# Kernel optimization log

Hardware: AMD Instinct MI355X
Metric: run time of the kernel (lower is better)

The kernel has to match this reference:

```python
import jax, jax.numpy as jnp
import numpy as np

# FUME epipolar image translation: for each output pixel p2=(x2,y2) the fundamental
# matrix F maps it to a line l = F @ [x2*d, y2*d, 1] in the input view (full-res
# coordinates; d = per-batch downsampling factor). The output value is the line
# integral of the input image along that epipolar line, computed by stepping one
# pixel at a time along the dominant axis with bilinear (1-D linear) interpolation
# across the other axis; out-of-bounds samples contribute zero.

def _translate(img, F, d):
    B, C, H, W = img.shape
    dt = img.dtype
    yy, xx = jnp.meshgrid(jnp.arange(H, dtype=dt), jnp.arange(W, dtype=dt), indexing='ij')
    db = d[:, None, None].astype(dt)                          # (B,1,1)
    px, py = xx[None] * db, yy[None] * db                     # (B,H,W) full-res coords
    a = F[0, 0] * px + F[0, 1] * py + F[0, 2]                 # line coeffs l = F @ [x,y,1]
    b = F[1, 0] * px + F[1, 1] * py + F[1, 2]
    c = F[2, 0] * px + F[2, 1] * py + F[2, 2]
    horiz = jnp.abs(b) >= jnp.abs(a)                          # dominant axis per pixel

    db4 = db[..., None]                                       # (B,1,1,1)
    # horizontal traversal: step over columns s, solve a*(s*d) + b*(y*d) + c = 0
    s = jnp.arange(W, dtype=dt)
    denom_h = jnp.where(horiz, b, jnp.ones((), dt))[..., None] * db4
    yline = -(a[..., None] * (s * db4) + c[..., None]) / denom_h    # (B,H,W,W)
    # vertical traversal: step over rows t, solve for x
    t = jnp.arange(H, dtype=dt)
    denom_v = jnp.where(horiz, jnp.ones((), dt), a)[..., None] * db4
    xline = -(b[..., None] * (t * db4) + c[..., None]) / denom_v    # (B,H,W,H)

    def sample_one(imgb, y, x):
        # imgb: (C,H,W); y: (H,W,W) row coord per column step; x: (H,W,H) col coord per row step
        y0 = jnp.floor(y)
        wy = y - y0
        y0i = jnp.clip(y0.astype(jnp.int32), 0, H - 1)
        y1i = jnp.clip(y0i + 1, 0, H - 1)
        cols = jnp.arange(W)
        vh = (1 - wy)[None] * imgb[:, y0i, cols] + wy[None] * imgb[:, y1i, cols]  # (C,H,W,W)
        vh = jnp.where(((y >= 0) & (y <= H - 1))[None], vh, jnp.zeros((), imgb.dtype)).sum(-1)

        x0 = jnp.floor(x)
        wx = x - x0
        x0i = jnp.clip(x0.astype(jnp.int32), 0, W - 1)
        x1i = jnp.clip(x0i + 1, 0, W - 1)
        rows = jnp.arange(H)
        vv = (1 - wx)[None] * imgb[:, rows, x0i] + wx[None] * imgb[:, rows, x1i]  # (C,H,W,H)
        vv = jnp.where(((x >= 0) & (x <= W - 1))[None], vv, jnp.zeros((), imgb.dtype)).sum(-1)
        return vh, vv

    vh, vv = jax.vmap(sample_one)(img, yline, xline)          # each (B,C,H,W)
    return jnp.where(horiz[:, None], vh, vv)


def setup_inputs() -> dict:
    key = jax.random.key(0)
    k1, k2, k3 = jax.random.split(key, 3)
    B, C, H, W = 4, 4, 128, 128
    view1 = jax.random.normal(k1, (B, C, H, W), jnp.float32)
    F21 = jax.random.normal(k2, (3, 3), jnp.float32)
    F12 = jax.random.normal(k3, (3, 3), jnp.float32)
    downsampled_factor = jnp.ones((B,), jnp.float32)
    return {"view1": view1, "F21": F21, "F12": F12, "downsampled_factor": downsampled_factor}


def reference(view1, F21, F12, downsampled_factor):
    # forward uses F21 only; F12 is kept for the backward pass in the original module
    return _translate(view1, F21, downsampled_factor)
```

## Files before the change

### kernel.cpp

```cpp
#include <hip/hip_runtime.h>


#define CC 4
#define HH 128
#define WW 128
#define LDK 128
#define CUBE (128 * LDK)

typedef _Float16 h2 __attribute__((ext_vector_type(2)));

__global__ void __launch_bounds__(256) fume_stage(
        const float* __restrict__ img, float4* __restrict__ ws) {
    __shared__ float tile[4][17][17];
    int x0 = blockIdx.x * 16, y0 = blockIdx.y * 16, b = blockIdx.z;
    int tx = threadIdx.x, ty = threadIdx.y;
    int id = ty * 16 + tx;
    const float* src = img + (size_t)b * CC * HH * WW;

    #pragma unroll
    for (int ch = 0; ch < 4; ++ch) {
        #pragma unroll
        for (int e = 0; e < 2; ++e) {
            int idx = id + e * 256;
            if (idx < 289) {
                int i = idx / 17, j = idx % 17;
                int r = min(y0 + i, HH - 1);
                int c = min(x0 + j, WW - 1);
                tile[ch][i][j] = src[(ch * HH + r) * WW + c];
            }
        }
    }
    __syncthreads();

    float4* base_h = ws + (size_t)b * (2 * CUBE);
    float4* base_v = base_h + CUBE;

    {
        h2 p0 = { (_Float16)tile[0][ty][tx], (_Float16)tile[0][ty + 1][tx] };
        h2 p1 = { (_Float16)tile[1][ty][tx], (_Float16)tile[1][ty + 1][tx] };
        h2 p2 = { (_Float16)tile[2][ty][tx], (_Float16)tile[2][ty + 1][tx] };
        h2 p3 = { (_Float16)tile[3][ty][tx], (_Float16)tile[3][ty + 1][tx] };
        float4 e = make_float4(__builtin_bit_cast(float, p0),
                               __builtin_bit_cast(float, p1),
                               __builtin_bit_cast(float, p2),
                               __builtin_bit_cast(float, p3));
        base_h[(y0 + ty) * LDK + (x0 + tx)] = e;
    }
    {
        h2 p0 = { (_Float16)tile[0][tx][ty], (_Float16)tile[0][tx][ty + 1] };
        h2 p1 = { (_Float16)tile[1][tx][ty], (_Float16)tile[1][tx][ty + 1] };
        h2 p2 = { (_Float16)tile[2][tx][ty], (_Float16)tile[2][tx][ty + 1] };
        h2 p3 = { (_Float16)tile[3][tx][ty], (_Float16)tile[3][tx][ty + 1] };
        float4 e = make_float4(__builtin_bit_cast(float, p0),
                               __builtin_bit_cast(float, p1),
                               __builtin_bit_cast(float, p2),
                               __builtin_bit_cast(float, p3));
        base_v[(x0 + ty) * LDK + (y0 + tx)] = e;
    }
}

__global__ void __launch_bounds__(512) fume_kernel(
        const float4* __restrict__ cubes,
        const float* __restrict__ F,
        const float* __restrict__ dsf,
        float* __restrict__ out) {
    int j = threadIdx.x;
    int w = threadIdx.y;
    int x = blockIdx.x * 8 + w;
    int y = blockIdx.y;
    int b = blockIdx.z;

    float d = dsf[b];
    float F00 = F[0], F01 = F[1], F02 = F[2];
    float F10 = F[3], F11 = F[4], F12 = F[5];
    float F20 = F[6], F21 = F[7], F22 = F[8];

    float px = __fmul_rn((float)x, d);
    float py = __fmul_rn((float)y, d);
    float av = __fadd_rn(__fadd_rn(__fmul_rn(F00, px), __fmul_rn(F01, py)), F02);
    float bv = __fadd_rn(__fadd_rn(__fmul_rn(F10, px), __fmul_rn(F11, py)), F12);
    float cv = __fadd_rn(__fadd_rn(__fmul_rn(F20, px), __fmul_rn(F21, py)), F22);

    bool horiz  = fabsf(bv) >= fabsf(av);
    float ncoef = horiz ? av : bv;
    float den   = __fmul_rn(horiz ? bv : av, d);
    float nrec  = -__fdiv_rn(1.0f, den);

    const float4* P = cubes + (size_t)b * (2 * CUBE) + (horiz ? 0 : CUBE);

    float A  = __fmul_rn(__fmul_rn(ncoef, d), nrec);
    float Bc = __fmul_rn(cv, nrec);
    int lkmin, lkmax;
    if (fabsf(A) > 1e-20f) {
        float inv = 1.0f / A;
        float k1 = (0.0f   - Bc) * inv;
        float k2 = (127.0f - Bc) * inv;
        float lo = fmaxf(fminf(k1, k2) - 2.0f, 0.0f);
        float hi = fminf(fmaxf(k1, k2) + 2.0f, 127.0f);
        if (lo > hi || !(lo == lo)) { lkmin = 1; lkmax = 0; }
        else { lkmin = (int)lo; lkmax = (int)hi; }
    } else {
        bool full = (Bc >= 0.0f) && (Bc <= 127.0f);
        lkmin = full ? 0 : 1;
        lkmax = full ? 127 : 0;
    }

    float a0 = 0.f, a1 = 0.f, a2 = 0.f, a3 = 0.f;
    #pragma unroll
    for (int t = 0; t < 2; ++t) {
        int k = lkmin + (t << 6) + j;
        if (k <= lkmax) {
            float m  = __fmul_rn((float)k, d);
            float q  = __fadd_rn(__fmul_rn(ncoef, m), cv);
            float u  = __fmul_rn(q, nrec);
            bool ok  = (u >= 0.f) && (u <= 127.f);
            int i0   = (int)floorf(u);
            i0 = max(0, min(i0, 126));
            float wq = __fsub_rn(u, (float)i0);
            h2 wp = __builtin_bit_cast(h2,
                        __builtin_amdgcn_cvt_pkrtz(__fsub_rn(1.f, wq), wq));
            wp = ok ? wp : (h2){(_Float16)0.f, (_Float16)0.f};
            float4 e = P[i0 * LDK + k];
            a0 = __builtin_amdgcn_fdot2(wp, __builtin_bit_cast(h2, e.x), a0, false);
            a1 = __builtin_amdgcn_fdot2(wp, __builtin_bit_cast(h2, e.y), a1, false);
            a2 = __builtin_amdgcn_fdot2(wp, __builtin_bit_cast(h2, e.z), a2, false);
            a3 = __builtin_amdgcn_fdot2(wp, __builtin_bit_cast(h2, e.w), a3, false);
        }
    }

    #pragma unroll
    for (int mlt = 32; mlt >= 1; mlt >>= 1) {
        a0 = __fadd_rn(a0, __shfl_xor(a0, mlt));
        a1 = __fadd_rn(a1, __shfl_xor(a1, mlt));
        a2 = __fadd_rn(a2, __shfl_xor(a2, mlt));
        a3 = __fadd_rn(a3, __shfl_xor(a3, mlt));
    }

    if (j < 4) {
        float v = (j == 0) ? a0 : (j == 1) ? a1 : (j == 2) ? a2 : a3;
        out[(((size_t)b * CC + j) * HH + y) * WW + x] = v;
    }
}

extern "C" void kernel_launch(void* const* d_in, const int* in_sizes, int n_in,
                              void* d_out, int out_size, void* d_ws, size_t ws_size,
                              hipStream_t stream) {
    const float* view1 = (const float*)d_in[0];
    const float* F21   = (const float*)d_in[1];
    const float* dsf   = (const float*)d_in[3];

    const int B = in_sizes[3];

    dim3 stb(16, 16, 1);
    dim3 stg(WW / 16, HH / 16, B);
    fume_stage<<<stg, stb, 0, stream>>>(view1, (float4*)d_ws);

    dim3 ftb(64, 8, 1);
    dim3 ftg(WW / 8, HH, B);
    fume_kernel<<<ftg, ftb, 0, stream>>>((const float4*)d_ws, F21, dsf,
                                         (float*)d_out);
}
```

Baseline: 79.32 us.

## Map eight output pixels per wavefront with 8-lane sub-groups and adaptive step count

Each wavefront now handles eight output pixels, with eight lanes per pixel, instead of one pixel per 64-lane wavefront. The loop runs only as many steps as the longest clipped line segment in the wave needs, and the final reduction spans eight lanes instead of 64. This is meant to cut idle lanes on short clipped segments and to shorten the shuffle reduction. In exchange the loop now has a runtime trip count, and lanes whose segments are short sit idle while the longest segment in the wave finishes; gathers from eight lanes may also coalesce less well.

```diff
diff --git a/kernel.cpp b/kernel.cpp
--- a/kernel.cpp
+++ b/kernel.cpp
@@ -64,9 +64,11 @@
         const float* __restrict__ F,
         const float* __restrict__ dsf,
         float* __restrict__ out) {
-    int j = threadIdx.x;
-    int w = threadIdx.y;
-    int x = blockIdx.x * 8 + w;
+    int lane = threadIdx.x;
+    int sub  = lane & 7;
+    int oct  = lane >> 3;
+    int w    = threadIdx.y;
+    int x = blockIdx.x * 64 + w * 8 + oct;
     int y = blockIdx.y;
     int b = blockIdx.z;
 
@@ -105,10 +107,15 @@
         lkmax = full ? 127 : 0;
     }
 
+    int len = lkmax - lkmin + 1;
+    int cnt = (len + 7) >> 3;
+    int wm  = cnt;
+    #pragma unroll
+    for (int m = 1; m < 64; m <<= 1) wm = max(wm, __shfl_xor(wm, m));
+
     float a0 = 0.f, a1 = 0.f, a2 = 0.f, a3 = 0.f;
-    #pragma unroll
-    for (int t = 0; t < 2; ++t) {
-        int k = lkmin + (t << 6) + j;
+    for (int s = 0; s < wm; ++s) {
+        int k = lkmin + (s << 3) + sub;
         if (k <= lkmax) {
             float m  = __fmul_rn((float)k, d);
             float q  = __fadd_rn(__fmul_rn(ncoef, m), cv);
@@ -129,16 +136,16 @@
     }
 
     #pragma unroll
-    for (int mlt = 32; mlt >= 1; mlt >>= 1) {
-        a0 = __fadd_rn(a0, __shfl_xor(a0, mlt));
-        a1 = __fadd_rn(a1, __shfl_xor(a1, mlt));
-        a2 = __fadd_rn(a2, __shfl_xor(a2, mlt));
-        a3 = __fadd_rn(a3, __shfl_xor(a3, mlt));
+    for (int m = 1; m < 8; m <<= 1) {
+        a0 = __fadd_rn(a0, __shfl_xor(a0, m));
+        a1 = __fadd_rn(a1, __shfl_xor(a1, m));
+        a2 = __fadd_rn(a2, __shfl_xor(a2, m));
+        a3 = __fadd_rn(a3, __shfl_xor(a3, m));
     }
 
-    if (j < 4) {
-        float v = (j == 0) ? a0 : (j == 1) ? a1 : (j == 2) ? a2 : a3;
-        out[(((size_t)b * CC + j) * HH + y) * WW + x] = v;
+    if (sub < 4) {
+        float v = (sub == 0) ? a0 : (sub == 1) ? a1 : (sub == 2) ? a2 : a3;
+        out[(((size_t)b * CC + sub) * HH + y) * WW + x] = v;
     }
 }
 
@@ -156,7 +163,7 @@
     fume_stage<<<stg, stb, 0, stream>>>(view1, (float4*)d_ws);
 
     dim3 ftb(64, 8, 1);
-    dim3 ftg(WW / 8, HH, B);
+    dim3 ftg(WW / 64, HH, B);
     fume_kernel<<<ftg, ftb, 0, stream>>>((const float4*)d_ws, F21, dsf,
                                          (float*)d_out);
 }
```

Result: faster. 69.57 us (-12.3%).
